# Kernel tuning notes

Measured on AMD Instinct MI355X. Metric: run time of the kernel, lower is better.

The kernel has to match this reference:

```python
import jax, jax.numpy as jnp
import numpy as np

N_HEADS = 4
D_HEAD = 32  # out_features // n_heads = 128 // 4
NEG_SLOPE = 0.2


def setup_inputs() -> dict:
    key = jax.random.key(0)
    k_x, k_adj, k_w, k_a = jax.random.split(key, 4)
    B, N, F_in, F_out = 4, 2048, 128, 128
    x = jax.random.normal(k_x, (B, N, F_in), dtype=jnp.float32)
    adj = jax.random.randint(k_adj, (B, N, N), 0, 2, dtype=jnp.int32)
    # Linear weight stored as [in, out] (torch stores [out, in]; math identical: x @ W)
    w_scale = np.sqrt(2.0 / (F_in + F_out))  # xavier-ish
    W = jax.random.normal(k_w, (F_in, F_out), dtype=jnp.float32) * w_scale
    a = jax.random.normal(k_a, (N_HEADS, 2 * D_HEAD), dtype=jnp.float32) * np.sqrt(2.0 / (2 * D_HEAD))
    return {"x": x, "adj": adj, "W": W, "a": a}


def reference(x, adj, W, a):
    B, N, _ = x.shape
    # project and split heads: [B, H, N, D]
    h = jnp.einsum('bnf,fo->bno', x, W).reshape(B, N, N_HEADS, D_HEAD).transpose(0, 2, 1, 3)
    # additive attention logits
    e_src = jnp.einsum('bhnd,hd->bhn', h, a[:, :D_HEAD])  # [B,H,N]
    e_dst = jnp.einsum('bhnd,hd->bhn', h, a[:, D_HEAD:])  # [B,H,N]
    e = e_src[:, :, :, None] + e_dst[:, :, None, :]       # [B,H,N,N]
    e = jnp.where(e > 0, e, NEG_SLOPE * e)                # leaky_relu(0.2)
    mask = (adj[:, None, :, :] == 0)                      # [B,1,N,N] -> broadcast over heads
    e = jnp.where(mask, -jnp.inf, e)
    alpha = jax.nn.softmax(e, axis=-1)                    # dropout omitted (eval mode)
    out = jnp.einsum('bhnm,bhmd->bhnd', alpha, h)         # weighted aggregation
    out = out.transpose(0, 2, 1, 3).reshape(B, N, N_HEADS * D_HEAD)
    return jax.nn.elu(out)
```

## Files before the change

### kernel.cpp

```cpp
#include <hip/hip_runtime.h>
#include <hip/hip_bf16.h>

#define BB 4
#define NN 2048
#define FIN 128
#define NH 4
#define DH 32
#define NS 0.2f
#define JP 2

typedef unsigned int u32;
typedef unsigned short u16;
typedef unsigned long long u64;
typedef __attribute__((ext_vector_type(8))) short short8;
typedef __attribute__((ext_vector_type(4))) float f32x4;
typedef __attribute__((ext_vector_type(4))) unsigned int u32x4;

#define OFF_ES   0
#define OFF_PQ   32768
#define OFF_HT   65536
#define OFF_BITS 589824
#define OFF_PACC 1114112
#define OFF_PS   3211264
#define PACC_STRIDE ((size_t)16 * NN * 32)
#define PS_STRIDE   ((size_t)16 * NN)

__device__ __forceinline__ u16 f2bf_rne(float f) {
  unsigned u = __float_as_uint(f);
  return (u16)((u + 0x7fffu + ((u >> 16) & 1u)) >> 16);
}

__device__ __forceinline__ int bitmask(u32 w, int e) {
#if __has_builtin(__builtin_amdgcn_sbfe)
  return __builtin_amdgcn_sbfe((int)w, e, 1);
#else
  return ((int)(w << (31 - e))) >> 31;
#endif
}

__global__ __launch_bounds__(256) void k_pack(const int* __restrict__ adj,
                                              u32* __restrict__ bits) {
  const int row = (blockIdx.x << 2) | (threadIdx.x >> 6);
  const int lane = threadIdx.x & 63;
  const int* src = adj + (size_t)row * NN;
  u32* dst = bits + (size_t)row * 64;
#pragma unroll 8
  for (int it = 0; it < 32; ++it) {
    const int v = src[it * 64 + lane];
    const u64 m = __ballot(v != 0);
    if (lane == 0) *(u64*)(dst + it * 2) = m;
  }
}

__global__ __launch_bounds__(256) void k_proj(
    const float* __restrict__ x, const float* __restrict__ W,
    const float* __restrict__ a, u16* __restrict__ hT,
    float* __restrict__ e_src, u32* __restrict__ PQ) {
  __shared__ float Ws[FIN * 128];
  const int tid = threadIdx.x;
  const int f = tid & 127, g = tid >> 7;
  const float4* Wg4 = (const float4*)W;
  float4* Ws4 = (float4*)Ws;
#pragma unroll
  for (int t = 0; t < 16; ++t) Ws4[t * 256 + tid] = Wg4[t * 256 + tid];
  __syncthreads();

  const int rb = blockIdx.x * 16 + g * 8;
  const int head = f >> 5, d = f & 31;
  const int b = rb >> 11, n0 = rb & (NN - 1);
  const int bh = b * NH + head;
  const float a_s = a[head * (2 * DH) + d];
  const float a_d = a[head * (2 * DH) + DH + d];

  float acc[8];
#pragma unroll
  for (int r = 0; r < 8; ++r) acc[r] = 0.f;

  const float* xb = x + (size_t)rb * FIN;
  for (int k = 0; k < FIN; ++k) {
    const float wv = Ws[k * 128 + f];
#pragma unroll
    for (int r = 0; r < 8; ++r) acc[r] = fmaf(wv, xb[r * FIN + k], acc[r]);
  }

  u16 hs[8];
#pragma unroll
  for (int r = 0; r < 8; ++r) hs[r] = f2bf_rne(acc[r]);
  u16* dst = hT + ((size_t)bh * DH + d) * NN + n0;
  *(int4*)dst = *(int4*)&hs[0];

#pragma unroll
  for (int r = 0; r < 8; ++r) {
    float s1 = acc[r] * a_s;
    float s2 = acc[r] * a_d;
#pragma unroll
    for (int off = 16; off >= 1; off >>= 1) {
      s1 += __shfl_xor(s1, off);
      s2 += __shfl_xor(s2, off);
    }
    if (d == 0) {
      e_src[(size_t)bh * NN + n0 + r] = s1;
      const u32 pb = f2bf_rne(__expf(s2));
      const u32 qb = f2bf_rne(__expf(NS * s2));
      PQ[(size_t)bh * NN + n0 + r] = (qb << 16) | pb;
    }
  }
}

__global__ __launch_bounds__(256) void k_attn(
    const u16* __restrict__ hT, const float* __restrict__ e_src,
    const u32* __restrict__ PQv, const u32* __restrict__ bits,
    float* __restrict__ pacc, float* __restrict__ pS) {
  __shared__ float part[4][32][33];
  __shared__ float sp[4][2][16];

  const int bid = blockIdx.x;
  const int jp = bid >> 10;
  const int bh = (bid >> 6) & 15;
  const int it = bid & 63;
  const int b = bh >> 2;

  const int w = threadIdx.x >> 6;
  const int lane = threadIdx.x & 63;
  const int lg = lane >> 4, lm = lane & 15;

  const int i0 = it * 32 + lm;
  const int i1 = i0 + 16;
  const float es0 = e_src[(size_t)bh * NN + i0];
  const float es1 = e_src[(size_t)bh * NN + i1];
  const float A0 = __expf(es0), B0 = __expf(NS * es0);
  const float A1 = __expf(es1), B1 = __expf(NS * es1);

  const int jwbase = jp * 1024 + w * 256;
  const u32* PQb = PQv + (size_t)bh * NN + jwbase;
  const u16* hb0 = hT + ((size_t)bh * DH + lm) * NN + jwbase;
  const u16* hb1 = hT + ((size_t)bh * DH + 16 + lm) * NN + jwbase;
  const int wbase = jwbase >> 5;
  const u32* br0 = bits + ((size_t)b * NN + i0) * 64 + wbase;
  const u32* br1 = bits + ((size_t)b * NN + i1) * 64 + wbase;
  const int shamt = lg * 8;
  const int jb = lg * 8;

  u32 wd0[8], wd1[8];
#pragma unroll
  for (int q = 0; q < 2; ++q) {
    const u32x4 v0 = *(const u32x4*)(br0 + q * 4);
    const u32x4 v1 = *(const u32x4*)(br1 + q * 4);
#pragma unroll
    for (int k2 = 0; k2 < 4; ++k2) { wd0[q * 4 + k2] = v0[k2]; wd1[q * 4 + k2] = v1[k2]; }
  }

  short8 ones;
#pragma unroll
  for (int e = 0; e < 8; ++e) ones[e] = (short)0x3F80;

  f32x4 acc00 = {0,0,0,0}, acc01 = {0,0,0,0};
  f32x4 acc10 = {0,0,0,0}, acc11 = {0,0,0,0};
  f32x4 accS0 = {0,0,0,0}, accS1 = {0,0,0,0};

#pragma unroll
  for (int t = 0; t < 8; ++t) {
    const int jj = t * 32 + jb;
    const u32x4 pqa = *(const u32x4*)(PQb + jj);
    const u32x4 pqb = *(const u32x4*)(PQb + jj + 4);
    const short8 hv0 = *(const short8*)(hb0 + jj);
    const short8 hv1 = *(const short8*)(hb1 + jj);
    const u32 wsh0 = wd0[t] >> shamt;
    const u32 wsh1 = wd1[t] >> shamt;
    short8 af0, af1;
#pragma unroll
    for (int e = 0; e < 8; ++e) {
      const u32 pq = (e < 4) ? pqa[e] : pqb[e - 4];
      const float Pf = __uint_as_float(pq << 16);
      const float Qf = __uint_as_float(pq & 0xffff0000u);
      const int m0 = bitmask(wsh0, e);
      const int m1 = bitmask(wsh1, e);
      float w0 = fmaxf(A0 * Pf, B0 * Qf);
      w0 = __int_as_float(__float_as_int(w0) & m0);
      af0[e] = (short)__builtin_bit_cast(unsigned short, __float2bfloat16(w0));
      float w1 = fmaxf(A1 * Pf, B1 * Qf);
      w1 = __int_as_float(__float_as_int(w1) & m1);
      af1[e] = (short)__builtin_bit_cast(unsigned short, __float2bfloat16(w1));
    }
    __builtin_amdgcn_s_setprio(1);
    acc00 = __builtin_amdgcn_mfma_f32_16x16x32_bf16(af0, hv0, acc00, 0, 0, 0);
    acc01 = __builtin_amdgcn_mfma_f32_16x16x32_bf16(af0, hv1, acc01, 0, 0, 0);
    acc10 = __builtin_amdgcn_mfma_f32_16x16x32_bf16(af1, hv0, acc10, 0, 0, 0);
    acc11 = __builtin_amdgcn_mfma_f32_16x16x32_bf16(af1, hv1, acc11, 0, 0, 0);
    accS0 = __builtin_amdgcn_mfma_f32_16x16x32_bf16(af0, ones, accS0, 0, 0, 0);
    accS1 = __builtin_amdgcn_mfma_f32_16x16x32_bf16(af1, ones, accS1, 0, 0, 0);
    __builtin_amdgcn_s_setprio(0);
  }

#pragma unroll
  for (int r = 0; r < 4; ++r) {
    const int rl = lg * 4 + r;
    part[w][rl][lm] = acc00[r];
    part[w][rl][16 + lm] = acc01[r];
    part[w][16 + rl][lm] = acc10[r];
    part[w][16 + rl][16 + lm] = acc11[r];
  }
  if (lm == 0) {
#pragma unroll
    for (int r = 0; r < 4; ++r) {
      sp[w][0][lg * 4 + r] = accS0[r];
      sp[w][1][lg * 4 + r] = accS1[r];
    }
  }
  __syncthreads();

  float* pa = pacc + ((size_t)jp * 16 + bh) * NN * 32;
  float* ps = pS + ((size_t)jp * 16 + bh) * NN;
  const int tid = threadIdx.x;
#pragma unroll
  for (int t = 0; t < 4; ++t) {
    const int idx = t * 256 + tid;
    const int row = idx >> 5, d = idx & 31;
    const float v = part[0][row][d] + part[1][row][d] +
                    part[2][row][d] + part[3][row][d];
    pa[(size_t)(it * 32 + row) * 32 + d] = v;
    if (d == 0) {
      const float s = sp[0][row >> 4][row & 15] + sp[1][row >> 4][row & 15] +
                      sp[2][row >> 4][row & 15] + sp[3][row >> 4][row & 15];
      ps[it * 32 + row] = s;
    }
  }
}

__global__ __launch_bounds__(256) void k_comb(
    const float* __restrict__ pacc, const float* __restrict__ pS,
    float* __restrict__ out) {
  const int idx = blockIdx.x * 256 + threadIdx.x;
  const int f = idx & 127;
  const int g = idx >> 7;
  const int b = g >> 11, n = g & (NN - 1);
  const int head = f >> 5, d = f & 31;
  const int bh = b * NH + head;
  const size_t base = ((size_t)bh * NN + n) * 32 + d;
  const size_t sbase = (size_t)bh * NN + n;
  float v = 0.f, s = 0.f;
#pragma unroll
  for (int p = 0; p < JP; ++p) {
    v += pacc[(size_t)p * PACC_STRIDE + base];
    s += pS[(size_t)p * PS_STRIDE + sbase];
  }
  const float o = v / s;
  out[idx] = o > 0.f ? o : (__expf(o) - 1.f);
}

extern "C" void kernel_launch(void* const* d_in, const int* in_sizes, int n_in,
                              void* d_out, int out_size, void* d_ws, size_t ws_size,
                              hipStream_t stream) {
  const float* x = (const float*)d_in[0];
  const int* adj = (const int*)d_in[1];
  const float* W = (const float*)d_in[2];
  const float* a = (const float*)d_in[3];
  float* out = (float*)d_out;
  float* ws = (float*)d_ws;

  float* e_src = ws + OFF_ES;
  u32* PQv = (u32*)(ws + OFF_PQ);
  u16* hT = (u16*)(ws + OFF_HT);
  u32* bits = (u32*)(ws + OFF_BITS);
  float* pacc = ws + OFF_PACC;
  float* pS = ws + OFF_PS;

  k_pack<<<(BB * NN) / 4, 256, 0, stream>>>(adj, bits);
  k_proj<<<(BB * NN) / 16, 256, 0, stream>>>(x, W, a, hT, e_src, PQv);
  k_attn<<<JP * BB * NH * 64, 256, 0, stream>>>(hT, e_src, PQv, bits, pacc, pS);
  k_comb<<<(BB * NN * 128) / 256, 256, 0, stream>>>(pacc, pS, out);
}
```

Before: 67.43 us.

## Fuse combine into attention, enlarge row tile, transpose packed adjacency bits

Removes the two-way split over the key dimension and the separate combine kernel. Each attention block now covers 64 query rows over all 2048 keys and applies normalization and ELU directly to the output. The adjacency bit-pack kernel now writes a word-major transposed layout through shared memory, so attention blocks can read mask words in a coalesced way per key tile. This avoids the partial-accumulator round trip through global memory and one launch. In exchange the grid shrinks to 512 blocks, each with more registers and a longer serial loop, which may hurt occupancy and load balance.

```diff
diff --git a/kernel.cpp b/kernel.cpp
--- a/kernel.cpp
+++ b/kernel.cpp
@@ -7,7 +7,6 @@
 #define NH 4
 #define DH 32
 #define NS 0.2f
-#define JP 2
 
 typedef unsigned int u32;
 typedef unsigned short u16;
@@ -20,10 +19,6 @@
 #define OFF_PQ   32768
 #define OFF_HT   65536
 #define OFF_BITS 589824
-#define OFF_PACC 1114112
-#define OFF_PS   3211264
-#define PACC_STRIDE ((size_t)16 * NN * 32)
-#define PS_STRIDE   ((size_t)16 * NN)
 
 __device__ __forceinline__ u16 f2bf_rne(float f) {
   unsigned u = __float_as_uint(f);
@@ -39,16 +34,35 @@
 }
 
 __global__ __launch_bounds__(256) void k_pack(const int* __restrict__ adj,
-                                              u32* __restrict__ bits) {
-  const int row = (blockIdx.x << 2) | (threadIdx.x >> 6);
+                                              u32* __restrict__ bitsT) {
+  __shared__ u32 tile[64][32];
+  const int row0 = blockIdx.x * 32;
+  const int w = threadIdx.x >> 6;
   const int lane = threadIdx.x & 63;
-  const int* src = adj + (size_t)row * NN;
-  u32* dst = bits + (size_t)row * 64;
-#pragma unroll 8
-  for (int it = 0; it < 32; ++it) {
-    const int v = src[it * 64 + lane];
-    const u64 m = __ballot(v != 0);
-    if (lane == 0) *(u64*)(dst + it * 2) = m;
+  const int b = row0 >> 11, n0 = row0 & (NN - 1);
+
+#pragma unroll
+  for (int r = 0; r < 8; ++r) {
+    const int rl = w * 8 + r;
+    const int* src = adj + (size_t)(row0 + rl) * NN;
+#pragma unroll 4
+    for (int it = 0; it < 32; ++it) {
+      const u64 m = __ballot(src[it * 64 + lane] != 0);
+      if (lane == 0) {
+        tile[2 * it][rl] = (u32)m;
+        tile[2 * it + 1][rl] = (u32)(m >> 32);
+      }
+    }
+  }
+  __syncthreads();
+
+  u32* dst = bitsT + (size_t)b * 64 * NN + n0;
+  const int tid = threadIdx.x;
+#pragma unroll
+  for (int t = 0; t < 8; ++t) {
+    const int idx = t * 256 + tid;
+    const int word = idx >> 5, rloc = idx & 31;
+    dst[(size_t)word * NN + rloc] = tile[word][rloc];
   }
 }
 
@@ -107,67 +121,62 @@
   }
 }
 
-__global__ __launch_bounds__(256) void k_attn(
+__global__ __launch_bounds__(256, 2) void k_attn(
     const u16* __restrict__ hT, const float* __restrict__ e_src,
-    const u32* __restrict__ PQv, const u32* __restrict__ bits,
-    float* __restrict__ pacc, float* __restrict__ pS) {
-  __shared__ float part[4][32][33];
-  __shared__ float sp[4][2][16];
+    const u32* __restrict__ PQv, const u32* __restrict__ bitsT,
+    float* __restrict__ out) {
+  __shared__ float part[4][64][33];
+  __shared__ float sp[4][4][16];
 
   const int bid = blockIdx.x;
-  const int jp = bid >> 10;
-  const int bh = (bid >> 6) & 15;
-  const int it = bid & 63;
-  const int b = bh >> 2;
+  const int bh = bid >> 5;
+  const int it = bid & 31;
+  const int b = bh >> 2, head = bh & 3;
 
   const int w = threadIdx.x >> 6;
   const int lane = threadIdx.x & 63;
   const int lg = lane >> 4, lm = lane & 15;
 
-  const int i0 = it * 32 + lm;
-  const int i1 = i0 + 16;
-  const float es0 = e_src[(size_t)bh * NN + i0];
-  const float es1 = e_src[(size_t)bh * NN + i1];
-  const float A0 = __expf(es0), B0 = __expf(NS * es0);
-  const float A1 = __expf(es1), B1 = __expf(NS * es1);
-
-  const int jwbase = jp * 1024 + w * 256;
+  float A[4], B[4];
+#pragma unroll
+  for (int rs = 0; rs < 4; ++rs) {
+    const float es = e_src[(size_t)bh * NN + it * 64 + rs * 16 + lm];
+    A[rs] = __expf(es);
+    B[rs] = __expf(NS * es);
+  }
+
+  const int jwbase = w * 512;
   const u32* PQb = PQv + (size_t)bh * NN + jwbase;
   const u16* hb0 = hT + ((size_t)bh * DH + lm) * NN + jwbase;
   const u16* hb1 = hT + ((size_t)bh * DH + 16 + lm) * NN + jwbase;
-  const int wbase = jwbase >> 5;
-  const u32* br0 = bits + ((size_t)b * NN + i0) * 64 + wbase;
-  const u32* br1 = bits + ((size_t)b * NN + i1) * 64 + wbase;
+  const u32* btb = bitsT + (size_t)b * 64 * NN + (size_t)(w * 16) * NN + it * 64 + lm;
   const int shamt = lg * 8;
   const int jb = lg * 8;
 
-  u32 wd0[8], wd1[8];
-#pragma unroll
-  for (int q = 0; q < 2; ++q) {
-    const u32x4 v0 = *(const u32x4*)(br0 + q * 4);
-    const u32x4 v1 = *(const u32x4*)(br1 + q * 4);
-#pragma unroll
-    for (int k2 = 0; k2 < 4; ++k2) { wd0[q * 4 + k2] = v0[k2]; wd1[q * 4 + k2] = v1[k2]; }
-  }
-
   short8 ones;
 #pragma unroll
   for (int e = 0; e < 8; ++e) ones[e] = (short)0x3F80;
 
   f32x4 acc00 = {0,0,0,0}, acc01 = {0,0,0,0};
   f32x4 acc10 = {0,0,0,0}, acc11 = {0,0,0,0};
+  f32x4 acc20 = {0,0,0,0}, acc21 = {0,0,0,0};
+  f32x4 acc30 = {0,0,0,0}, acc31 = {0,0,0,0};
   f32x4 accS0 = {0,0,0,0}, accS1 = {0,0,0,0};
-
-#pragma unroll
-  for (int t = 0; t < 8; ++t) {
+  f32x4 accS2 = {0,0,0,0}, accS3 = {0,0,0,0};
+
+#pragma unroll 4
+  for (int t = 0; t < 16; ++t) {
     const int jj = t * 32 + jb;
     const u32x4 pqa = *(const u32x4*)(PQb + jj);
     const u32x4 pqb = *(const u32x4*)(PQb + jj + 4);
     const short8 hv0 = *(const short8*)(hb0 + jj);
     const short8 hv1 = *(const short8*)(hb1 + jj);
-    const u32 wsh0 = wd0[t] >> shamt;
-    const u32 wsh1 = wd1[t] >> shamt;
-    short8 af0, af1;
+    const u32* btw = btb + (size_t)t * NN;
+    const u32 wsh0 = btw[0] >> shamt;
+    const u32 wsh1 = btw[16] >> shamt;
+    const u32 wsh2 = btw[32] >> shamt;
+    const u32 wsh3 = btw[48] >> shamt;
+    short8 af0, af1, af2, af3;
 #pragma unroll
     for (int e = 0; e < 8; ++e) {
       const u32 pq = (e < 4) ? pqa[e] : pqb[e - 4];
@@ -175,77 +184,72 @@
       const float Qf = __uint_as_float(pq & 0xffff0000u);
       const int m0 = bitmask(wsh0, e);
       const int m1 = bitmask(wsh1, e);
-      float w0 = fmaxf(A0 * Pf, B0 * Qf);
+      const int m2 = bitmask(wsh2, e);
+      const int m3 = bitmask(wsh3, e);
+      float w0 = fmaxf(A[0] * Pf, B[0] * Qf);
+      float w1 = fmaxf(A[1] * Pf, B[1] * Qf);
+      float w2 = fmaxf(A[2] * Pf, B[2] * Qf);
+      float w3 = fmaxf(A[3] * Pf, B[3] * Qf);
       w0 = __int_as_float(__float_as_int(w0) & m0);
+      w1 = __int_as_float(__float_as_int(w1) & m1);
+      w2 = __int_as_float(__float_as_int(w2) & m2);
+      w3 = __int_as_float(__float_as_int(w3) & m3);
       af0[e] = (short)__builtin_bit_cast(unsigned short, __float2bfloat16(w0));
-      float w1 = fmaxf(A1 * Pf, B1 * Qf);
-      w1 = __int_as_float(__float_as_int(w1) & m1);
       af1[e] = (short)__builtin_bit_cast(unsigned short, __float2bfloat16(w1));
-    }
-    __builtin_amdgcn_s_setprio(1);
+      af2[e] = (short)__builtin_bit_cast(unsigned short, __float2bfloat16(w2));
+      af3[e] = (short)__builtin_bit_cast(unsigned short, __float2bfloat16(w3));
+    }
     acc00 = __builtin_amdgcn_mfma_f32_16x16x32_bf16(af0, hv0, acc00, 0, 0, 0);
     acc01 = __builtin_amdgcn_mfma_f32_16x16x32_bf16(af0, hv1, acc01, 0, 0, 0);
     acc10 = __builtin_amdgcn_mfma_f32_16x16x32_bf16(af1, hv0, acc10, 0, 0, 0);
     acc11 = __builtin_amdgcn_mfma_f32_16x16x32_bf16(af1, hv1, acc11, 0, 0, 0);
+    acc20 = __builtin_amdgcn_mfma_f32_16x16x32_bf16(af2, hv0, acc20, 0, 0, 0);
+    acc21 = __builtin_amdgcn_mfma_f32_16x16x32_bf16(af2, hv1, acc21, 0, 0, 0);
+    acc30 = __builtin_amdgcn_mfma_f32_16x16x32_bf16(af3, hv0, acc30, 0, 0, 0);
+    acc31 = __builtin_amdgcn_mfma_f32_16x16x32_bf16(af3, hv1, acc31, 0, 0, 0);
     accS0 = __builtin_amdgcn_mfma_f32_16x16x32_bf16(af0, ones, accS0, 0, 0, 0);
     accS1 = __builtin_amdgcn_mfma_f32_16x16x32_bf16(af1, ones, accS1, 0, 0, 0);
-    __builtin_amdgcn_s_setprio(0);
+    accS2 = __builtin_amdgcn_mfma_f32_16x16x32_bf16(af2, ones, accS2, 0, 0, 0);
+    accS3 = __builtin_amdgcn_mfma_f32_16x16x32_bf16(af3, ones, accS3, 0, 0, 0);
   }
 
 #pragma unroll
   for (int r = 0; r < 4; ++r) {
     const int rl = lg * 4 + r;
-    part[w][rl][lm] = acc00[r];
-    part[w][rl][16 + lm] = acc01[r];
-    part[w][16 + rl][lm] = acc10[r];
+    part[w][rl][lm]           = acc00[r];
+    part[w][rl][16 + lm]      = acc01[r];
+    part[w][16 + rl][lm]      = acc10[r];
     part[w][16 + rl][16 + lm] = acc11[r];
+    part[w][32 + rl][lm]      = acc20[r];
+    part[w][32 + rl][16 + lm] = acc21[r];
+    part[w][48 + rl][lm]      = acc30[r];
+    part[w][48 + rl][16 + lm] = acc31[r];
   }
   if (lm == 0) {
 #pragma unroll
     for (int r = 0; r < 4; ++r) {
       sp[w][0][lg * 4 + r] = accS0[r];
       sp[w][1][lg * 4 + r] = accS1[r];
+      sp[w][2][lg * 4 + r] = accS2[r];
+      sp[w][3][lg * 4 + r] = accS3[r];
     }
   }
   __syncthreads();
 
-  float* pa = pacc + ((size_t)jp * 16 + bh) * NN * 32;
-  float* ps = pS + ((size_t)jp * 16 + bh) * NN;
   const int tid = threadIdx.x;
 #pragma unroll
-  for (int t = 0; t < 4; ++t) {
+  for (int t = 0; t < 8; ++t) {
     const int idx = t * 256 + tid;
     const int row = idx >> 5, d = idx & 31;
     const float v = part[0][row][d] + part[1][row][d] +
                     part[2][row][d] + part[3][row][d];
-    pa[(size_t)(it * 32 + row) * 32 + d] = v;
-    if (d == 0) {
-      const float s = sp[0][row >> 4][row & 15] + sp[1][row >> 4][row & 15] +
-                      sp[2][row >> 4][row & 15] + sp[3][row >> 4][row & 15];
-      ps[it * 32 + row] = s;
-    }
-  }
-}
-
-__global__ __launch_bounds__(256) void k_comb(
-    const float* __restrict__ pacc, const float* __restrict__ pS,
-    float* __restrict__ out) {
-  const int idx = blockIdx.x * 256 + threadIdx.x;
-  const int f = idx & 127;
-  const int g = idx >> 7;
-  const int b = g >> 11, n = g & (NN - 1);
-  const int head = f >> 5, d = f & 31;
-  const int bh = b * NH + head;
-  const size_t base = ((size_t)bh * NN + n) * 32 + d;
-  const size_t sbase = (size_t)bh * NN + n;
-  float v = 0.f, s = 0.f;
-#pragma unroll
-  for (int p = 0; p < JP; ++p) {
-    v += pacc[(size_t)p * PACC_STRIDE + base];
-    s += pS[(size_t)p * PS_STRIDE + sbase];
-  }
-  const float o = v / s;
-  out[idx] = o > 0.f ? o : (__expf(o) - 1.f);
+    const float s = sp[0][row >> 4][row & 15] + sp[1][row >> 4][row & 15] +
+                    sp[2][row >> 4][row & 15] + sp[3][row >> 4][row & 15];
+    const float o = v / s;
+    const int n = it * 64 + row;
+    out[((size_t)b * NN + n) * 128 + head * 32 + d] =
+        o > 0.f ? o : (__expf(o) - 1.f);
+  }
 }
 
 extern "C" void kernel_launch(void* const* d_in, const int* in_sizes, int n_in,
@@ -261,12 +265,9 @@
   float* e_src = ws + OFF_ES;
   u32* PQv = (u32*)(ws + OFF_PQ);
   u16* hT = (u16*)(ws + OFF_HT);
-  u32* bits = (u32*)(ws + OFF_BITS);
-  float* pacc = ws + OFF_PACC;
-  float* pS = ws + OFF_PS;
-
-  k_pack<<<(BB * NN) / 4, 256, 0, stream>>>(adj, bits);
+  u32* bitsT = (u32*)(ws + OFF_BITS);
+
+  k_pack<<<(BB * NN) / 32, 256, 0, stream>>>(adj, bitsT);
   k_proj<<<(BB * NN) / 16, 256, 0, stream>>>(x, W, a, hT, e_src, PQv);
-  k_attn<<<JP * BB * NH * 64, 256, 0, stream>>>(hT, e_src, PQv, bits, pacc, pS);
-  k_comb<<<(BB * NN * 128) / 256, 256, 0, stream>>>(pacc, pS, out);
-}
+  k_attn<<<BB * NH * 32, 256, 0, stream>>>(hT, e_src, PQv, bitsT, out);
+}
```

Result: slower. 119.2 us (+76.8%).
